# Performance work log

Measured on AMD Instinct MI355X. Metric: run time of the kernel, lower is better.

## Reference

```python
import jax, jax.numpy as jnp
import numpy as np

BN_EPS = 1e-5


def setup_inputs() -> dict:
    key = jax.random.key(0)
    ks = jax.random.split(key, 10)
    B, C, N = 16, 512, 4096
    Cr = C // 4
    s = 0.05
    return {
        "x": jax.random.normal(ks[0], (B, C, N), dtype=jnp.float32),
        # channel attention MLP (1x1 convs on pooled vector)
        "w1": jax.random.normal(ks[1], (Cr, C), dtype=jnp.float32) * s,
        "b1": jnp.zeros((Cr,), jnp.float32),
        "w2": jax.random.normal(ks[2], (C, Cr), dtype=jnp.float32) * s,
        "b2": jnp.zeros((C,), jnp.float32),
        # spatial attention branch
        "w3": jax.random.normal(ks[3], (Cr, C), dtype=jnp.float32) * s,
        "b3": jnp.zeros((Cr,), jnp.float32),
        "bn_gamma": jnp.ones((Cr,), jnp.float32),
        "bn_beta": jnp.zeros((Cr,), jnp.float32),
        "bn_mean": jnp.zeros((Cr,), jnp.float32),
        "bn_var": jnp.ones((Cr,), jnp.float32),
        "w4": jax.random.normal(ks[4], (1, Cr), dtype=jnp.float32) * s,
        "b4": jnp.zeros((1,), jnp.float32),
    }


def reference(x, w1, b1, w2, b2, w3, b3, bn_gamma, bn_beta, bn_mean, bn_var, w4, b4):
    # x: [B, C, N]; inference semantics (Dropout = identity, BN uses running stats)
    # ---- channel attention ----
    pooled = jnp.mean(x, axis=-1)                        # [B, C] (AdaptiveAvgPool1d(1))
    h = jax.nn.relu(pooled @ w1.T + b1)                  # [B, C/4]
    ca = jax.nn.sigmoid(h @ w2.T + b2)[:, :, None]       # [B, C, 1]
    x_ca = x * ca                                        # [B, C, N]
    # ---- spatial attention ----
    h2 = jnp.einsum('oc,bcn->bon', w3, x_ca) + b3[:, None]    # [B, C/4, N]
    inv = bn_gamma / jnp.sqrt(bn_var + BN_EPS)                 # [C/4]
    h2 = h2 * inv[:, None] + (bn_beta - bn_mean * inv)[:, None]
    h2 = jax.nn.relu(h2)
    sa = jax.nn.sigmoid(jnp.einsum('oc,bcn->bon', w4, h2) + b4[:, None])  # [B, 1, N]
    return x + x_ca * sa
```

## Files before the change

### kernel.cpp

```cpp
#include <hip/hip_runtime.h>
#include <math.h>

constexpr int B  = 16;
constexpr int C  = 512;
constexpr int N  = 4096;
constexpr int CR = 128;
constexpr int NT = 128;
constexpr int KC = 64;

typedef __attribute__((ext_vector_type(8))) short bf16x8;
typedef __attribute__((ext_vector_type(4))) float f32x4;

__device__ __forceinline__ float sigmoidf_(float v) {
    return 1.0f / (1.0f + __expf(-v));
}
__device__ __forceinline__ unsigned f2bf(float f) {
    unsigned u = __float_as_uint(f);
    u += 0x7fffu + ((u >> 16) & 1u);
    return u >> 16;
}

#define LGKM_BARRIER() do {                                   \
    asm volatile("s_waitcnt lgkmcnt(0)" ::: "memory");        \
    __builtin_amdgcn_s_barrier();                             \
    asm volatile("" ::: "memory");                            \
} while (0)

__global__ __launch_bounds__(256) void k_pre(
    const float* __restrict__ x, float* __restrict__ pooled,
    const float* __restrict__ w3, const float* __restrict__ b3,
    const float* __restrict__ gamma, const float* __restrict__ beta,
    const float* __restrict__ mean, const float* __restrict__ var,
    unsigned short* __restrict__ w3f, float* __restrict__ bias2)
{
    if (blockIdx.x < 2048) {
        int w    = threadIdx.x >> 6;
        int lane = threadIdx.x & 63;
        int row  = blockIdx.x * 4 + w;
        const float4* xr = (const float4*)(x + (size_t)row * N);
        float s = 0.f;
        #pragma unroll
        for (int i = 0; i < 16; ++i) {
            float4 v = xr[i * 64 + lane];
            s += v.x + v.y + v.z + v.w;
        }
        #pragma unroll
        for (int off = 32; off; off >>= 1) s += __shfl_xor(s, off, 64);
        if (lane == 0) pooled[row] = s * (1.0f / N);
    } else {
        int idx  = (blockIdx.x - 2048) * 256 + threadIdx.x;
        int g    = idx >> 6;
        int lane = idx & 63;
        int ck   = g >> 4;
        int kk   = (g >> 3) & 1;
        int ob   = g & 7;
        int o    = ob * 16 + (lane & 15);
        int c    = ck * 64 + kk * 32 + (lane >> 4) * 8;
        float inv = gamma[o] * rsqrtf(var[o] + 1e-5f);
        float4 a  = *(const float4*)(w3 + o * C + c);
        float4 bq = *(const float4*)(w3 + o * C + c + 4);
        unsigned r0 = f2bf(a.x * inv)  | (f2bf(a.y * inv) << 16);
        unsigned r1 = f2bf(a.z * inv)  | (f2bf(a.w * inv) << 16);
        unsigned r2 = f2bf(bq.x * inv) | (f2bf(bq.y * inv) << 16);
        unsigned r3 = f2bf(bq.z * inv) | (f2bf(bq.w * inv) << 16);
        *(uint4*)((char*)w3f + (size_t)idx * 16) = make_uint4(r0, r1, r2, r3);
        if (idx < CR) {
            float iv = gamma[idx] * rsqrtf(var[idx] + 1e-5f);
            bias2[idx] = b3[idx] * iv + beta[idx] - mean[idx] * iv;
        }
    }
}

__global__ __launch_bounds__(128) void k_ca(
    const float* __restrict__ pooled,
    const float* __restrict__ w1, const float* __restrict__ b1,
    const float* __restrict__ w2, const float* __restrict__ b2,
    float* __restrict__ ca)
{
    __shared__ float ps[C];
    __shared__ float hs[CR];
    int b = blockIdx.x, t = threadIdx.x;
    #pragma unroll
    for (int i = 0; i < 4; ++i) ps[t + i * 128] = pooled[b * C + t + i * 128];
    __syncthreads();

    float acc = b1[t];
    const float4* wr = (const float4*)(w1 + t * C);
    const float4* pr = (const float4*)ps;
    #pragma unroll 4
    for (int i = 0; i < C / 4; ++i) {
        float4 wv = wr[i], pv = pr[i];
        acc += wv.x * pv.x + wv.y * pv.y + wv.z * pv.z + wv.w * pv.w;
    }
    hs[t] = fmaxf(acc, 0.f);
    __syncthreads();

    #pragma unroll
    for (int k = 0; k < 4; ++k) {
        int c2 = t + k * 128;
        float a = b2[c2];
        const float4* w2r = (const float4*)(w2 + c2 * CR);
        const float4* hr  = (const float4*)hs;
        #pragma unroll 4
        for (int i = 0; i < CR / 4; ++i) {
            float4 wv = w2r[i], hv = hr[i];
            a += wv.x * hv.x + wv.y * hv.y + wv.z * hv.z + wv.w * hv.w;
        }
        ca[b * C + c2] = sigmoidf_(a);
    }
}

__global__ __launch_bounds__(512, 2) void k_main(
    const float* __restrict__ x, const float* __restrict__ ca,
    const unsigned short* __restrict__ w3f, const float* __restrict__ bias2,
    const float* __restrict__ w4, const float* __restrict__ b4,
    float* __restrict__ out)
{
    __shared__ __align__(16) short lds_x[2][NT * KC];
    __shared__ float ca_s[C];
    __shared__ __align__(16) float sa_s[NT];
    __shared__ float red[4][NT];
    __shared__ float bias2_s[CR];
    __shared__ float w4_s[CR];

    const int t    = threadIdx.x;
    const int lane = t & 63;
    const int w    = t >> 6;
    const int b    = blockIdx.y;
    const int n0   = blockIdx.x * NT;
    const int wo   = (w & 3) * 32;
    const int wn   = (w >> 2) * 64;
    const int ob0  = (w & 3) * 2;

    const size_t xbase = (size_t)b * C * N + n0;
    const int ng = t & 63;
    const int cg = t >> 6;

    float2 xva[8], xvb[8];

#define LOADX(dst, CK) do { const int c0_ = (CK) * KC;                         \
    _Pragma("unroll") for (int ci = 0; ci < 8; ++ci)                           \
        dst[ci] = *(const float2*)(x + xbase + (size_t)(c0_ + cg * 8 + ci) * N + 2 * ng); \
} while (0)

#define CONVERT_WRITE(src, CK, BUF) do { const int c0_ = (CK) * KC;            \
    unsigned q0[4], q1[4];                                                     \
    _Pragma("unroll") for (int h = 0; h < 4; ++h) {                            \
        float s0 = ca_s[c0_ + cg * 8 + 2 * h];                                 \
        float s1 = ca_s[c0_ + cg * 8 + 2 * h + 1];                             \
        q0[h] = f2bf(src[2 * h].x * s0) | (f2bf(src[2 * h + 1].x * s1) << 16); \
        q1[h] = f2bf(src[2 * h].y * s0) | (f2bf(src[2 * h + 1].y * s1) << 16); \
    }                                                                          \
    int nl0 = 2 * ng, nl1 = 2 * ng + 1;                                        \
    int a0 = (nl0 * 128 + cg * 16) ^ ((nl0 & 7) << 4);                         \
    int a1 = (nl1 * 128 + cg * 16) ^ ((nl1 & 7) << 4);                         \
    *(uint4*)((char*)lds_x[BUF] + a0) = make_uint4(q0[0], q0[1], q0[2], q0[3]);\
    *(uint4*)((char*)lds_x[BUF] + a1) = make_uint4(q1[0], q1[1], q1[2], q1[3]);\
} while (0)

    LOADX(xva, 0);
    LOADX(xvb, 1);

    ca_s[t] = ca[b * C + t];
    if (t < CR) { bias2_s[t] = bias2[t]; w4_s[t] = w4[t]; }
    LGKM_BARRIER();

    CONVERT_WRITE(xva, 0, 0);

    f32x4 acc[2][4];
    #pragma unroll
    for (int i = 0; i < 2; ++i)
        #pragma unroll
        for (int j = 0; j < 4; ++j) acc[i][j] = (f32x4)0.f;

    const char* wf = (const char*)w3f;

    #pragma unroll
    for (int ck = 0; ck < 8; ++ck) {
        if (ck < 6) { if (ck & 1) LOADX(xvb, ck + 2); else LOADX(xva, ck + 2); }

        LGKM_BARRIER();

        #pragma unroll
        for (int kk = 0; kk < 2; ++kk) {
            bf16x8 af[2];
            #pragma unroll
            for (int i = 0; i < 2; ++i) {
                int g = ck * 16 + kk * 8 + ob0 + i;
                af[i] = *(const bf16x8*)(wf + (size_t)(g * 64 + lane) * 16);
            }
            bf16x8 bfr[4];
            #pragma unroll
            for (int j = 0; j < 4; ++j) {
                int br = wn + j * 16 + (lane & 15);
                int bb = (br * 128 + kk * 64 + (lane >> 4) * 16) ^ ((br & 7) << 4);
                bfr[j] = *(const bf16x8*)((const char*)lds_x[ck & 1] + bb);
            }
            #pragma unroll
            for (int i = 0; i < 2; ++i)
                #pragma unroll
                for (int j = 0; j < 4; ++j)
                    acc[i][j] = __builtin_amdgcn_mfma_f32_16x16x32_bf16(af[i], bfr[j], acc[i][j], 0, 0, 0);
        }
        if (ck < 7) { if (ck & 1) CONVERT_WRITE(xva, ck + 1, 0); else CONVERT_WRITE(xvb, ck + 1, 1); }
    }

    #pragma unroll
    for (int j = 0; j < 4; ++j) {
        float p = 0.f;
        #pragma unroll
        for (int i = 0; i < 2; ++i) {
            #pragma unroll
            for (int r = 0; r < 4; ++r) {
                int o = wo + i * 16 + ((lane >> 4) << 2) + r;
                p = fmaf(w4_s[o], fmaxf(acc[i][j][r] + bias2_s[o], 0.f), p);
            }
        }
        p += __shfl_xor(p, 16, 64);
        p += __shfl_xor(p, 32, 64);
        if (lane < 16) red[w & 3][wn + j * 16 + lane] = p;
    }
    __syncthreads();
    if (t < NT) sa_s[t] = sigmoidf_(red[0][t] + red[1][t] + red[2][t] + red[3][t] + b4[0]);
    __syncthreads();

    #pragma unroll 4
    for (int it = 0; it < 32; ++it) {
        int f4 = it * 512 + t;
        int c  = f4 >> 5;
        int n4 = f4 & 31;
        size_t off = xbase + (size_t)c * N + n4 * 4;
        float4 v = *(const float4*)(x + off);
        float cav = ca_s[c];
        float4 sv = *(const float4*)&sa_s[n4 * 4];
        float4 o4;
        o4.x = v.x * fmaf(cav, sv.x, 1.0f);
        o4.y = v.y * fmaf(cav, sv.y, 1.0f);
        o4.z = v.z * fmaf(cav, sv.z, 1.0f);
        o4.w = v.w * fmaf(cav, sv.w, 1.0f);
        *(float4*)(out + off) = o4;
    }
#undef LOADX
#undef CONVERT_WRITE
}

extern "C" void kernel_launch(void* const* d_in, const int* in_sizes, int n_in,
                              void* d_out, int out_size, void* d_ws, size_t ws_size,
                              hipStream_t stream)
{
    const float* x   = (const float*)d_in[0];
    const float* w1  = (const float*)d_in[1];
    const float* b1  = (const float*)d_in[2];
    const float* w2  = (const float*)d_in[3];
    const float* b2  = (const float*)d_in[4];
    const float* w3  = (const float*)d_in[5];
    const float* b3  = (const float*)d_in[6];
    const float* g   = (const float*)d_in[7];
    const float* be  = (const float*)d_in[8];
    const float* mn  = (const float*)d_in[9];
    const float* vr  = (const float*)d_in[10];
    const float* w4  = (const float*)d_in[11];
    const float* b4  = (const float*)d_in[12];
    float* out = (float*)d_out;

    float* ws     = (float*)d_ws;
    float* pooled = ws;
    float* ca     = ws + 8192;
    float* bias2  = ws + 16384;
    unsigned short* w3f = (unsigned short*)(ws + 16640);

    k_pre<<<2048 + 32, 256, 0, stream>>>(x, pooled, w3, b3, g, be, mn, vr, w3f, bias2);
    k_ca<<<B, 128, 0, stream>>>(pooled, w1, b1, w2, b2, ca);
    dim3 g3(N / NT, B);
    k_main<<<g3, 512, 0, stream>>>(x, ca, w3f, bias2, w4, b4, out);
}
```

Baseline: 121.2 us.

## Fold channel attention into per-batch W3 and split output pass into separate kernel

The channel-attention scale is folded into a per-batch bf16 copy of the BN-scaled W3 inside k_ca, so the GEMM kernel converts raw x to bf16 without multiplying by ca. The final elementwise output pass moves out of the GEMM kernel into a separate streaming kernel that reads a stored sa vector. This removes per-element ca multiplies and LDS lookups from the GEMM inner loop and frees the GEMM kernel from the output tail. In exchange it adds a kernel launch, a 2 MB per-batch weight buffer, and an extra sa round trip through global memory. The bf16 rounding order also changes slightly.

```diff
diff --git a/kernel.cpp b/kernel.cpp
--- a/kernel.cpp
+++ b/kernel.cpp
@@ -71,33 +71,37 @@
     }
 }
 
-__global__ __launch_bounds__(128) void k_ca(
+__global__ __launch_bounds__(256) void k_ca(
     const float* __restrict__ pooled,
     const float* __restrict__ w1, const float* __restrict__ b1,
     const float* __restrict__ w2, const float* __restrict__ b2,
-    float* __restrict__ ca)
+    const unsigned short* __restrict__ w3f,
+    float* __restrict__ ca, unsigned short* __restrict__ w3b)
 {
     __shared__ float ps[C];
     __shared__ float hs[CR];
+    __shared__ float ca_s[C];
     int b = blockIdx.x, t = threadIdx.x;
+    ps[t] = pooled[b * C + t];
+    ps[t + 256] = pooled[b * C + t + 256];
+    __syncthreads();
+
+    if (t < CR) {
+        float acc = b1[t];
+        const float4* wr = (const float4*)(w1 + t * C);
+        const float4* pr = (const float4*)ps;
+        #pragma unroll 4
+        for (int i = 0; i < C / 4; ++i) {
+            float4 wv = wr[i], pv = pr[i];
+            acc += wv.x * pv.x + wv.y * pv.y + wv.z * pv.z + wv.w * pv.w;
+        }
+        hs[t] = fmaxf(acc, 0.f);
+    }
+    __syncthreads();
+
     #pragma unroll
-    for (int i = 0; i < 4; ++i) ps[t + i * 128] = pooled[b * C + t + i * 128];
-    __syncthreads();
-
-    float acc = b1[t];
-    const float4* wr = (const float4*)(w1 + t * C);
-    const float4* pr = (const float4*)ps;
-    #pragma unroll 4
-    for (int i = 0; i < C / 4; ++i) {
-        float4 wv = wr[i], pv = pr[i];
-        acc += wv.x * pv.x + wv.y * pv.y + wv.z * pv.z + wv.w * pv.w;
-    }
-    hs[t] = fmaxf(acc, 0.f);
-    __syncthreads();
-
-    #pragma unroll
-    for (int k = 0; k < 4; ++k) {
-        int c2 = t + k * 128;
+    for (int k = 0; k < 2; ++k) {
+        int c2 = t + k * 256;
         float a = b2[c2];
         const float4* w2r = (const float4*)(w2 + c2 * CR);
         const float4* hr  = (const float4*)hs;
@@ -106,19 +110,49 @@
             float4 wv = w2r[i], hv = hr[i];
             a += wv.x * hv.x + wv.y * hv.y + wv.z * hv.z + wv.w * hv.w;
         }
-        ca[b * C + c2] = sigmoidf_(a);
-    }
-}
-
-__global__ __launch_bounds__(512, 2) void k_main(
-    const float* __restrict__ x, const float* __restrict__ ca,
-    const unsigned short* __restrict__ w3f, const float* __restrict__ bias2,
-    const float* __restrict__ w4, const float* __restrict__ b4,
-    float* __restrict__ out)
+        float cav = sigmoidf_(a);
+        ca_s[c2] = cav;
+        ca[b * C + c2] = cav;
+    }
+    __syncthreads();
+
+    #pragma unroll 4
+    for (int j = 0; j < 32; ++j) {
+        int i    = j * 256 + t;
+        int g    = i >> 6;
+        int lane = i & 63;
+        int ck   = g >> 4;
+        int kk   = (g >> 3) & 1;
+        int c0   = ck * 64 + kk * 32 + ((lane >> 4) << 3);
+        uint4 wv = *(const uint4*)((const char*)w3f + (size_t)i * 16);
+        const float* cb = &ca_s[c0];
+        uint4 ov;
+        {
+            float lo = __uint_as_float(wv.x << 16), hi = __uint_as_float(wv.x & 0xffff0000u);
+            ov.x = f2bf(lo * cb[0]) | (f2bf(hi * cb[1]) << 16);
+        }
+        {
+            float lo = __uint_as_float(wv.y << 16), hi = __uint_as_float(wv.y & 0xffff0000u);
+            ov.y = f2bf(lo * cb[2]) | (f2bf(hi * cb[3]) << 16);
+        }
+        {
+            float lo = __uint_as_float(wv.z << 16), hi = __uint_as_float(wv.z & 0xffff0000u);
+            ov.z = f2bf(lo * cb[4]) | (f2bf(hi * cb[5]) << 16);
+        }
+        {
+            float lo = __uint_as_float(wv.w << 16), hi = __uint_as_float(wv.w & 0xffff0000u);
+            ov.w = f2bf(lo * cb[6]) | (f2bf(hi * cb[7]) << 16);
+        }
+        *(uint4*)((char*)w3b + ((size_t)b * 8192 + i) * 16) = ov;
+    }
+}
+
+__global__ __launch_bounds__(512, 2) void k_gemm(
+    const float* __restrict__ x, const unsigned short* __restrict__ w3b,
+    const float* __restrict__ bias2, const float* __restrict__ w4,
+    const float* __restrict__ b4, float* __restrict__ sa)
 {
     __shared__ __align__(16) short lds_x[2][NT * KC];
-    __shared__ float ca_s[C];
-    __shared__ __align__(16) float sa_s[NT];
     __shared__ float red[4][NT];
     __shared__ float bias2_s[CR];
     __shared__ float w4_s[CR];
@@ -136,6 +170,8 @@
     const int ng = t & 63;
     const int cg = t >> 6;
 
+    if (t < CR) { bias2_s[t] = bias2[t]; w4_s[t] = w4[t]; }
+
     float2 xva[8], xvb[8];
 
 #define LOADX(dst, CK) do { const int c0_ = (CK) * KC;                         \
@@ -143,13 +179,11 @@
         dst[ci] = *(const float2*)(x + xbase + (size_t)(c0_ + cg * 8 + ci) * N + 2 * ng); \
 } while (0)
 
-#define CONVERT_WRITE(src, CK, BUF) do { const int c0_ = (CK) * KC;            \
+#define CONVERT_WRITE(src, BUF) do {                                           \
     unsigned q0[4], q1[4];                                                     \
     _Pragma("unroll") for (int h = 0; h < 4; ++h) {                            \
-        float s0 = ca_s[c0_ + cg * 8 + 2 * h];                                 \
-        float s1 = ca_s[c0_ + cg * 8 + 2 * h + 1];                             \
-        q0[h] = f2bf(src[2 * h].x * s0) | (f2bf(src[2 * h + 1].x * s1) << 16); \
-        q1[h] = f2bf(src[2 * h].y * s0) | (f2bf(src[2 * h + 1].y * s1) << 16); \
+        q0[h] = f2bf(src[2 * h].x) | (f2bf(src[2 * h + 1].x) << 16);           \
+        q1[h] = f2bf(src[2 * h].y) | (f2bf(src[2 * h + 1].y) << 16);           \
     }                                                                          \
     int nl0 = 2 * ng, nl1 = 2 * ng + 1;                                        \
     int a0 = (nl0 * 128 + cg * 16) ^ ((nl0 & 7) << 4);                         \
@@ -160,12 +194,7 @@
 
     LOADX(xva, 0);
     LOADX(xvb, 1);
-
-    ca_s[t] = ca[b * C + t];
-    if (t < CR) { bias2_s[t] = bias2[t]; w4_s[t] = w4[t]; }
-    LGKM_BARRIER();
-
-    CONVERT_WRITE(xva, 0, 0);
+    CONVERT_WRITE(xva, 0);
 
     f32x4 acc[2][4];
     #pragma unroll
@@ -173,7 +202,7 @@
         #pragma unroll
         for (int j = 0; j < 4; ++j) acc[i][j] = (f32x4)0.f;
 
-    const char* wf = (const char*)w3f;
+    const char* wb = (const char*)w3b + (size_t)b * 131072;
 
     #pragma unroll
     for (int ck = 0; ck < 8; ++ck) {
@@ -187,7 +216,7 @@
             #pragma unroll
             for (int i = 0; i < 2; ++i) {
                 int g = ck * 16 + kk * 8 + ob0 + i;
-                af[i] = *(const bf16x8*)(wf + (size_t)(g * 64 + lane) * 16);
+                af[i] = *(const bf16x8*)(wb + (size_t)(g * 64 + lane) * 16);
             }
             bf16x8 bfr[4];
             #pragma unroll
@@ -202,7 +231,7 @@
                 for (int j = 0; j < 4; ++j)
                     acc[i][j] = __builtin_amdgcn_mfma_f32_16x16x32_bf16(af[i], bfr[j], acc[i][j], 0, 0, 0);
         }
-        if (ck < 7) { if (ck & 1) CONVERT_WRITE(xva, ck + 1, 0); else CONVERT_WRITE(xvb, ck + 1, 1); }
+        if (ck < 7) { if (ck & 1) CONVERT_WRITE(xva, 0); else CONVERT_WRITE(xvb, 1); }
     }
 
     #pragma unroll
@@ -221,27 +250,36 @@
         if (lane < 16) red[w & 3][wn + j * 16 + lane] = p;
     }
     __syncthreads();
-    if (t < NT) sa_s[t] = sigmoidf_(red[0][t] + red[1][t] + red[2][t] + red[3][t] + b4[0]);
-    __syncthreads();
-
-    #pragma unroll 4
-    for (int it = 0; it < 32; ++it) {
-        int f4 = it * 512 + t;
-        int c  = f4 >> 5;
-        int n4 = f4 & 31;
-        size_t off = xbase + (size_t)c * N + n4 * 4;
-        float4 v = *(const float4*)(x + off);
-        float cav = ca_s[c];
-        float4 sv = *(const float4*)&sa_s[n4 * 4];
-        float4 o4;
-        o4.x = v.x * fmaf(cav, sv.x, 1.0f);
-        o4.y = v.y * fmaf(cav, sv.y, 1.0f);
-        o4.z = v.z * fmaf(cav, sv.z, 1.0f);
-        o4.w = v.w * fmaf(cav, sv.w, 1.0f);
-        *(float4*)(out + off) = o4;
-    }
+    if (t < NT)
+        sa[b * N + n0 + t] = sigmoidf_(red[0][t] + red[1][t] + red[2][t] + red[3][t] + b4[0]);
 #undef LOADX
 #undef CONVERT_WRITE
+}
+
+__global__ __launch_bounds__(256) void k_out(
+    const float* __restrict__ x, const float* __restrict__ ca,
+    const float* __restrict__ sa, float* __restrict__ out)
+{
+    const float4* x4  = (const float4*)x;
+    const float4* sa4 = (const float4*)sa;
+    float4* o4        = (float4*)out;
+    int base = blockIdx.x * 256 + threadIdx.x;
+    #pragma unroll 4
+    for (int it = 0; it < 16; ++it) {
+        int i4 = base + it * 524288;
+        float4 v  = x4[i4];
+        int b  = i4 >> 19;
+        int c  = (i4 >> 10) & 511;
+        int n4 = i4 & 1023;
+        float cav = ca[b * 512 + c];
+        float4 sv = sa4[b * 1024 + n4];
+        float4 r;
+        r.x = v.x * fmaf(cav, sv.x, 1.0f);
+        r.y = v.y * fmaf(cav, sv.y, 1.0f);
+        r.z = v.z * fmaf(cav, sv.z, 1.0f);
+        r.w = v.w * fmaf(cav, sv.w, 1.0f);
+        o4[i4] = r;
+    }
 }
 
 extern "C" void kernel_launch(void* const* d_in, const int* in_sizes, int n_in,
@@ -268,9 +306,12 @@
     float* ca     = ws + 8192;
     float* bias2  = ws + 16384;
     unsigned short* w3f = (unsigned short*)(ws + 16640);
+    unsigned short* w3b = (unsigned short*)(ws + 49408);
+    float* sa     = ws + 573696;
 
     k_pre<<<2048 + 32, 256, 0, stream>>>(x, pooled, w3, b3, g, be, mn, vr, w3f, bias2);
-    k_ca<<<B, 128, 0, stream>>>(pooled, w1, b1, w2, b2, ca);
+    k_ca<<<B, 256, 0, stream>>>(pooled, w1, b1, w2, b2, w3f, ca, w3b);
     dim3 g3(N / NT, B);
-    k_main<<<g3, 512, 0, stream>>>(x, ca, w3f, bias2, w4, b4, out);
-}
+    k_gemm<<<g3, 512, 0, stream>>>(x, w3b, bias2, w4, b4, sa);
+    k_out<<<2048, 256, 0, stream>>>(x, ca, sa, out);
+}
```

New measurement: 124.9 us, median of 2. 3.0% more time.

## Fold channel attention into per-batch weights and pre-transpose x to bf16

Applied to the files above, without the earlier changes.

The pooling pass now also writes a transposed bf16 copy of x laid out in MFMA fragment order. The channel-attention kernel folds the ca scale into a per-batch copy of the bf16 w3 weights. The main GEMM then streams both operands straight from global memory, with no LDS staging or per-tile conversion, and targets higher occupancy. This trades an extra 64 MB write plus a re-read of that buffer for removing the in-loop x conversion and barriers. A fallback path is kept for when the workspace is too small.

```diff
diff --git a/kernel.cpp b/kernel.cpp
--- a/kernel.cpp
+++ b/kernel.cpp
@@ -31,24 +31,51 @@
     const float* __restrict__ w3, const float* __restrict__ b3,
     const float* __restrict__ gamma, const float* __restrict__ beta,
     const float* __restrict__ mean, const float* __restrict__ var,
-    unsigned short* __restrict__ w3f, float* __restrict__ bias2)
+    unsigned short* __restrict__ w3f, float* __restrict__ bias2,
+    unsigned short* __restrict__ xbT, int do_xbt)
 {
-    if (blockIdx.x < 2048) {
-        int w    = threadIdx.x >> 6;
-        int lane = threadIdx.x & 63;
-        int row  = blockIdx.x * 4 + w;
-        const float4* xr = (const float4*)(x + (size_t)row * N);
-        float s = 0.f;
-        #pragma unroll
-        for (int i = 0; i < 16; ++i) {
-            float4 v = xr[i * 64 + lane];
-            s += v.x + v.y + v.z + v.w;
-        }
-        #pragma unroll
-        for (int off = 32; off; off >>= 1) s += __shfl_xor(s, off, 64);
-        if (lane == 0) pooled[row] = s * (1.0f / N);
+    if (blockIdx.x < 512) {
+        __shared__ float tr[16][256];
+        const int g = blockIdx.x, b = g >> 5, c16 = g & 31;
+        const int t = threadIdx.x, lane = t & 63, w = t >> 6;
+        const float4* xr = (const float4*)(x + ((size_t)b * C + c16 * 16) * N);
+        float ps[4] = {0.f, 0.f, 0.f, 0.f};
+        for (int ch = 0; ch < 16; ++ch) {
+            float4 v[4];
+            #pragma unroll
+            for (int i = 0; i < 4; ++i) {
+                int r = i * 4 + w;
+                v[i] = xr[(size_t)r * 1024 + ch * 64 + lane];
+                ps[i] += v[i].x + v[i].y + v[i].z + v[i].w;
+            }
+            if (do_xbt) {
+                #pragma unroll
+                for (int i = 0; i < 4; ++i)
+                    *(float4*)&tr[i * 4 + w][lane * 4] = v[i];
+                __syncthreads();
+                int n = ch * 256 + t;
+                unsigned q[8];
+                #pragma unroll
+                for (int h = 0; h < 8; ++h)
+                    q[h] = f2bf(tr[2 * h][t]) | (f2bf(tr[2 * h + 1][t]) << 16);
+                size_t off = (((size_t)b * 32 + c16) * 4096 + n) * 16;
+                *(uint4*)(xbT + off)     = make_uint4(q[0], q[1], q[2], q[3]);
+                *(uint4*)(xbT + off + 8) = make_uint4(q[4], q[5], q[6], q[7]);
+                __syncthreads();
+            }
+        }
+        #pragma unroll
+        for (int i = 0; i < 4; ++i) {
+            #pragma unroll
+            for (int o = 32; o; o >>= 1) ps[i] += __shfl_xor(ps[i], o, 64);
+        }
+        if (lane == 0) {
+            #pragma unroll
+            for (int i = 0; i < 4; ++i)
+                pooled[b * C + c16 * 16 + i * 4 + w] = ps[i] * (1.0f / N);
+        }
     } else {
-        int idx  = (blockIdx.x - 2048) * 256 + threadIdx.x;
+        int idx  = (blockIdx.x - 512) * 256 + threadIdx.x;
         int g    = idx >> 6;
         int lane = idx & 63;
         int ck   = g >> 4;
@@ -71,33 +98,37 @@
     }
 }
 
-__global__ __launch_bounds__(128) void k_ca(
+__global__ __launch_bounds__(256) void k_ca(
     const float* __restrict__ pooled,
     const float* __restrict__ w1, const float* __restrict__ b1,
     const float* __restrict__ w2, const float* __restrict__ b2,
-    float* __restrict__ ca)
+    const unsigned short* __restrict__ w3f,
+    float* __restrict__ ca, unsigned short* __restrict__ w3b)
 {
     __shared__ float ps[C];
     __shared__ float hs[CR];
+    __shared__ float ca_s[C];
     int b = blockIdx.x, t = threadIdx.x;
-    #pragma unroll
-    for (int i = 0; i < 4; ++i) ps[t + i * 128] = pooled[b * C + t + i * 128];
-    __syncthreads();
-
-    float acc = b1[t];
-    const float4* wr = (const float4*)(w1 + t * C);
-    const float4* pr = (const float4*)ps;
-    #pragma unroll 4
-    for (int i = 0; i < C / 4; ++i) {
-        float4 wv = wr[i], pv = pr[i];
-        acc += wv.x * pv.x + wv.y * pv.y + wv.z * pv.z + wv.w * pv.w;
-    }
-    hs[t] = fmaxf(acc, 0.f);
-    __syncthreads();
-
-    #pragma unroll
-    for (int k = 0; k < 4; ++k) {
-        int c2 = t + k * 128;
+    ps[t] = pooled[b * C + t];
+    ps[t + 256] = pooled[b * C + t + 256];
+    __syncthreads();
+
+    if (t < CR) {
+        float acc = b1[t];
+        const float4* wr = (const float4*)(w1 + t * C);
+        const float4* pr = (const float4*)ps;
+        #pragma unroll 4
+        for (int i = 0; i < C / 4; ++i) {
+            float4 wv = wr[i], pv = pr[i];
+            acc += wv.x * pv.x + wv.y * pv.y + wv.z * pv.z + wv.w * pv.w;
+        }
+        hs[t] = fmaxf(acc, 0.f);
+    }
+    __syncthreads();
+
+    #pragma unroll
+    for (int k = 0; k < 2; ++k) {
+        int c2 = t + k * 256;
         float a = b2[c2];
         const float4* w2r = (const float4*)(w2 + c2 * CR);
         const float4* hr  = (const float4*)hs;
@@ -106,20 +137,52 @@
             float4 wv = w2r[i], hv = hr[i];
             a += wv.x * hv.x + wv.y * hv.y + wv.z * hv.z + wv.w * hv.w;
         }
-        ca[b * C + c2] = sigmoidf_(a);
-    }
-}
-
-__global__ __launch_bounds__(512, 2) void k_main(
-    const float* __restrict__ x, const float* __restrict__ ca,
-    const unsigned short* __restrict__ w3f, const float* __restrict__ bias2,
-    const float* __restrict__ w4, const float* __restrict__ b4,
-    float* __restrict__ out)
+        float cav = sigmoidf_(a);
+        ca_s[c2] = cav;
+        ca[b * C + c2] = cav;
+    }
+    __syncthreads();
+
+    #pragma unroll 4
+    for (int j = 0; j < 32; ++j) {
+        int i    = j * 256 + t;
+        int g    = i >> 6;
+        int lane = i & 63;
+        int ck   = g >> 4;
+        int kk   = (g >> 3) & 1;
+        int c0   = ck * 64 + kk * 32 + ((lane >> 4) << 3);
+        uint4 wv = *(const uint4*)((const char*)w3f + (size_t)i * 16);
+        const float* cb = &ca_s[c0];
+        uint4 ov;
+        {
+            float lo = __uint_as_float(wv.x << 16), hi = __uint_as_float(wv.x & 0xffff0000u);
+            ov.x = f2bf(lo * cb[0]) | (f2bf(hi * cb[1]) << 16);
+        }
+        {
+            float lo = __uint_as_float(wv.y << 16), hi = __uint_as_float(wv.y & 0xffff0000u);
+            ov.y = f2bf(lo * cb[2]) | (f2bf(hi * cb[3]) << 16);
+        }
+        {
+            float lo = __uint_as_float(wv.z << 16), hi = __uint_as_float(wv.z & 0xffff0000u);
+            ov.z = f2bf(lo * cb[4]) | (f2bf(hi * cb[5]) << 16);
+        }
+        {
+            float lo = __uint_as_float(wv.w << 16), hi = __uint_as_float(wv.w & 0xffff0000u);
+            ov.w = f2bf(lo * cb[6]) | (f2bf(hi * cb[7]) << 16);
+        }
+        *(uint4*)((char*)w3b + ((size_t)b * 8192 + i) * 16) = ov;
+    }
+}
+
+__global__ __launch_bounds__(512, 4) void k_gemm_out(
+    const float* __restrict__ x, const unsigned short* __restrict__ xbT,
+    const unsigned short* __restrict__ w3b, const float* __restrict__ ca,
+    const float* __restrict__ bias2, const float* __restrict__ w4,
+    const float* __restrict__ b4, float* __restrict__ out)
 {
-    __shared__ __align__(16) short lds_x[2][NT * KC];
+    __shared__ float red[4][NT];
+    __shared__ __align__(16) float sa_s[NT];
     __shared__ float ca_s[C];
-    __shared__ __align__(16) float sa_s[NT];
-    __shared__ float red[4][NT];
     __shared__ float bias2_s[CR];
     __shared__ float w4_s[CR];
 
@@ -132,40 +195,15 @@
     const int wn   = (w >> 2) * 64;
     const int ob0  = (w & 3) * 2;
 
-    const size_t xbase = (size_t)b * C * N + n0;
-    const int ng = t & 63;
-    const int cg = t >> 6;
-
-    float2 xva[8], xvb[8];
-
-#define LOADX(dst, CK) do { const int c0_ = (CK) * KC;                         \
-    _Pragma("unroll") for (int ci = 0; ci < 8; ++ci)                           \
-        dst[ci] = *(const float2*)(x + xbase + (size_t)(c0_ + cg * 8 + ci) * N + 2 * ng); \
-} while (0)
-
-#define CONVERT_WRITE(src, CK, BUF) do { const int c0_ = (CK) * KC;            \
-    unsigned q0[4], q1[4];                                                     \
-    _Pragma("unroll") for (int h = 0; h < 4; ++h) {                            \
-        float s0 = ca_s[c0_ + cg * 8 + 2 * h];                                 \
-        float s1 = ca_s[c0_ + cg * 8 + 2 * h + 1];                             \
-        q0[h] = f2bf(src[2 * h].x * s0) | (f2bf(src[2 * h + 1].x * s1) << 16); \
-        q1[h] = f2bf(src[2 * h].y * s0) | (f2bf(src[2 * h + 1].y * s1) << 16); \
-    }                                                                          \
-    int nl0 = 2 * ng, nl1 = 2 * ng + 1;                                        \
-    int a0 = (nl0 * 128 + cg * 16) ^ ((nl0 & 7) << 4);                         \
-    int a1 = (nl1 * 128 + cg * 16) ^ ((nl1 & 7) << 4);                         \
-    *(uint4*)((char*)lds_x[BUF] + a0) = make_uint4(q0[0], q0[1], q0[2], q0[3]);\
-    *(uint4*)((char*)lds_x[BUF] + a1) = make_uint4(q1[0], q1[1], q1[2], q1[3]);\
-} while (0)
-
-    LOADX(xva, 0);
-    LOADX(xvb, 1);
-
-    ca_s[t] = ca[b * C + t];
-    if (t < CR) { bias2_s[t] = bias2[t]; w4_s[t] = w4[t]; }
-    LGKM_BARRIER();
-
-    CONVERT_WRITE(xva, 0, 0);
+    if (t < 256) { ca_s[t] = ca[b * C + t]; ca_s[t + 256] = ca[b * C + t + 256]; }
+    if (t < CR)  { bias2_s[t] = bias2[t]; w4_s[t] = w4[t]; }
+
+    const int csel = lane >> 4;
+    const unsigned short* bbase = xbT
+        + ((size_t)b * 32 + (csel >> 1)) * 65536
+        + (size_t)(n0 + wn + (lane & 15)) * 16
+        + (csel & 1) * 8;
+    const char* wb = (const char*)w3b + (size_t)b * 131072 + (size_t)lane * 16;
 
     f32x4 acc[2][4];
     #pragma unroll
@@ -173,36 +211,27 @@
         #pragma unroll
         for (int j = 0; j < 4; ++j) acc[i][j] = (f32x4)0.f;
 
-    const char* wf = (const char*)w3f;
-
     #pragma unroll
     for (int ck = 0; ck < 8; ++ck) {
-        if (ck < 6) { if (ck & 1) LOADX(xvb, ck + 2); else LOADX(xva, ck + 2); }
-
-        LGKM_BARRIER();
-
-        #pragma unroll
-        for (int kk = 0; kk < 2; ++kk) {
-            bf16x8 af[2];
-            #pragma unroll
-            for (int i = 0; i < 2; ++i) {
-                int g = ck * 16 + kk * 8 + ob0 + i;
-                af[i] = *(const bf16x8*)(wf + (size_t)(g * 64 + lane) * 16);
-            }
-            bf16x8 bfr[4];
-            #pragma unroll
-            for (int j = 0; j < 4; ++j) {
-                int br = wn + j * 16 + (lane & 15);
-                int bb = (br * 128 + kk * 64 + (lane >> 4) * 16) ^ ((br & 7) << 4);
-                bfr[j] = *(const bf16x8*)((const char*)lds_x[ck & 1] + bb);
-            }
+        bf16x8 af[2][2];
+        #pragma unroll
+        for (int kk = 0; kk < 2; ++kk)
+            #pragma unroll
+            for (int i = 0; i < 2; ++i)
+                af[kk][i] = *(const bf16x8*)(wb + (size_t)(ck * 16 + kk * 8 + ob0 + i) * 1024);
+        bf16x8 bfv[2][4];
+        #pragma unroll
+        for (int kk = 0; kk < 2; ++kk)
+            #pragma unroll
+            for (int j = 0; j < 4; ++j)
+                bfv[kk][j] = *(const bf16x8*)(bbase + (size_t)(ck * 4 + kk * 2) * 65536 + j * 256);
+        #pragma unroll
+        for (int kk = 0; kk < 2; ++kk)
             #pragma unroll
             for (int i = 0; i < 2; ++i)
                 #pragma unroll
                 for (int j = 0; j < 4; ++j)
-                    acc[i][j] = __builtin_amdgcn_mfma_f32_16x16x32_bf16(af[i], bfr[j], acc[i][j], 0, 0, 0);
-        }
-        if (ck < 7) { if (ck & 1) CONVERT_WRITE(xva, ck + 1, 0); else CONVERT_WRITE(xvb, ck + 1, 1); }
+                    acc[i][j] = __builtin_amdgcn_mfma_f32_16x16x32_bf16(af[kk][i], bfv[kk][j], acc[i][j], 0, 0, 0);
     }
 
     #pragma unroll
@@ -221,9 +250,11 @@
         if (lane < 16) red[w & 3][wn + j * 16 + lane] = p;
     }
     __syncthreads();
-    if (t < NT) sa_s[t] = sigmoidf_(red[0][t] + red[1][t] + red[2][t] + red[3][t] + b4[0]);
-    __syncthreads();
-
+    if (t < NT)
+        sa_s[t] = sigmoidf_(red[0][t] + red[1][t] + red[2][t] + red[3][t] + b4[0]);
+    __syncthreads();
+
+    const size_t xbase = (size_t)b * C * N + n0;
     #pragma unroll 4
     for (int it = 0; it < 32; ++it) {
         int f4 = it * 512 + t;
@@ -240,8 +271,136 @@
         o4.w = v.w * fmaf(cav, sv.w, 1.0f);
         *(float4*)(out + off) = o4;
     }
+}
+
+__global__ __launch_bounds__(512, 2) void k_main_fb(
+    const float* __restrict__ x, const float* __restrict__ ca,
+    const unsigned short* __restrict__ w3f, const float* __restrict__ bias2,
+    const float* __restrict__ w4, const float* __restrict__ b4,
+    float* __restrict__ out)
+{
+    __shared__ __align__(16) short lds_x[2][NT * KC];
+    __shared__ float ca_s[C];
+    __shared__ __align__(16) float sa_s[NT];
+    __shared__ float red[4][NT];
+    __shared__ float bias2_s[CR];
+    __shared__ float w4_s[CR];
+
+    const int t    = threadIdx.x;
+    const int lane = t & 63;
+    const int w    = t >> 6;
+    const int b    = blockIdx.y;
+    const int n0   = blockIdx.x * NT;
+    const int wo   = (w & 3) * 32;
+    const int wn   = (w >> 2) * 64;
+    const int ob0  = (w & 3) * 2;
+
+    const size_t xbase = (size_t)b * C * N + n0;
+    const int ng = t & 63;
+    const int cg = t >> 6;
+
+    ca_s[t] = ca[b * C + t];
+    if (t < CR) { bias2_s[t] = bias2[t]; w4_s[t] = w4[t]; }
+
+    float2 xva[8], xvb[8];
+
+#define LOADX(dst, CK) do { const int c0_ = (CK) * KC;                         \
+    _Pragma("unroll") for (int ci = 0; ci < 8; ++ci)                           \
+        dst[ci] = *(const float2*)(x + xbase + (size_t)(c0_ + cg * 8 + ci) * N + 2 * ng); \
+} while (0)
+#define CONVERT_WRITE(src, CK, BUF) do { const int c0_ = (CK) * KC;            \
+    unsigned q0[4], q1[4];                                                     \
+    _Pragma("unroll") for (int h = 0; h < 4; ++h) {                            \
+        float s0 = ca_s[c0_ + cg * 8 + 2 * h];                                 \
+        float s1 = ca_s[c0_ + cg * 8 + 2 * h + 1];                             \
+        q0[h] = f2bf(src[2 * h].x * s0) | (f2bf(src[2 * h + 1].x * s1) << 16); \
+        q1[h] = f2bf(src[2 * h].y * s0) | (f2bf(src[2 * h + 1].y * s1) << 16); \
+    }                                                                          \
+    int nl0 = 2 * ng, nl1 = 2 * ng + 1;                                        \
+    int a0 = (nl0 * 128 + cg * 16) ^ ((nl0 & 7) << 4);                         \
+    int a1 = (nl1 * 128 + cg * 16) ^ ((nl1 & 7) << 4);                         \
+    *(uint4*)((char*)lds_x[BUF] + a0) = make_uint4(q0[0], q0[1], q0[2], q0[3]);\
+    *(uint4*)((char*)lds_x[BUF] + a1) = make_uint4(q1[0], q1[1], q1[2], q1[3]);\
+} while (0)
+
+    LOADX(xva, 0);
+    LOADX(xvb, 1);
+    LGKM_BARRIER();
+    CONVERT_WRITE(xva, 0, 0);
+
+    f32x4 acc[2][4];
+    #pragma unroll
+    for (int i = 0; i < 2; ++i)
+        #pragma unroll
+        for (int j = 0; j < 4; ++j) acc[i][j] = (f32x4)0.f;
+
+    const char* wf = (const char*)w3f;
+
+    #pragma unroll
+    for (int ck = 0; ck < 8; ++ck) {
+        if (ck < 6) { if (ck & 1) LOADX(xvb, ck + 2); else LOADX(xva, ck + 2); }
+        LGKM_BARRIER();
+        #pragma unroll
+        for (int kk = 0; kk < 2; ++kk) {
+            bf16x8 af[2];
+            #pragma unroll
+            for (int i = 0; i < 2; ++i) {
+                int g = ck * 16 + kk * 8 + ob0 + i;
+                af[i] = *(const bf16x8*)(wf + (size_t)(g * 64 + lane) * 16);
+            }
+            bf16x8 bfr[4];
+            #pragma unroll
+            for (int j = 0; j < 4; ++j) {
+                int br = wn + j * 16 + (lane & 15);
+                int bb = (br * 128 + kk * 64 + (lane >> 4) * 16) ^ ((br & 7) << 4);
+                bfr[j] = *(const bf16x8*)((const char*)lds_x[ck & 1] + bb);
+            }
+            #pragma unroll
+            for (int i = 0; i < 2; ++i)
+                #pragma unroll
+                for (int j = 0; j < 4; ++j)
+                    acc[i][j] = __builtin_amdgcn_mfma_f32_16x16x32_bf16(af[i], bfr[j], acc[i][j], 0, 0, 0);
+        }
+        if (ck < 7) { if (ck & 1) CONVERT_WRITE(xva, ck + 1, 0); else CONVERT_WRITE(xvb, ck + 1, 1); }
+    }
 #undef LOADX
 #undef CONVERT_WRITE
+
+    #pragma unroll
+    for (int j = 0; j < 4; ++j) {
+        float p = 0.f;
+        #pragma unroll
+        for (int i = 0; i < 2; ++i) {
+            #pragma unroll
+            for (int r = 0; r < 4; ++r) {
+                int o = wo + i * 16 + ((lane >> 4) << 2) + r;
+                p = fmaf(w4_s[o], fmaxf(acc[i][j][r] + bias2_s[o], 0.f), p);
+            }
+        }
+        p += __shfl_xor(p, 16, 64);
+        p += __shfl_xor(p, 32, 64);
+        if (lane < 16) red[w & 3][wn + j * 16 + lane] = p;
+    }
+    __syncthreads();
+    if (t < NT) sa_s[t] = sigmoidf_(red[0][t] + red[1][t] + red[2][t] + red[3][t] + b4[0]);
+    __syncthreads();
+
+    #pragma unroll 4
+    for (int it = 0; it < 32; ++it) {
+        int f4 = it * 512 + t;
+        int c  = f4 >> 5;
+        int n4 = f4 & 31;
+        size_t off = xbase + (size_t)c * N + n4 * 4;
+        float4 v = *(const float4*)(x + off);
+        float cav = ca_s[c];
+        float4 sv = *(const float4*)&sa_s[n4 * 4];
+        float4 o4;
+        o4.x = v.x * fmaf(cav, sv.x, 1.0f);
+        o4.y = v.y * fmaf(cav, sv.y, 1.0f);
+        o4.z = v.z * fmaf(cav, sv.z, 1.0f);
+        o4.w = v.w * fmaf(cav, sv.w, 1.0f);
+        *(float4*)(out + off) = o4;
+    }
 }
 
 extern "C" void kernel_launch(void* const* d_in, const int* in_sizes, int n_in,
@@ -268,9 +427,18 @@
     float* ca     = ws + 8192;
     float* bias2  = ws + 16384;
     unsigned short* w3f = (unsigned short*)(ws + 16640);
-
-    k_pre<<<2048 + 32, 256, 0, stream>>>(x, pooled, w3, b3, g, be, mn, vr, w3f, bias2);
-    k_ca<<<B, 128, 0, stream>>>(pooled, w1, b1, w2, b2, ca);
+    unsigned short* w3b = (unsigned short*)(ws + 49408);
+    unsigned short* xbT = (unsigned short*)(ws + 573696);
+
+    const size_t need = (size_t)573696 * 4 + (size_t)B * C * N * 2;
+    const int use_xbt = (ws_size >= need) ? 1 : 0;
+
+    k_pre<<<512 + 32, 256, 0, stream>>>(x, pooled, w3, b3, g, be, mn, vr,
+                                        w3f, bias2, xbT, use_xbt);
+    k_ca<<<B, 256, 0, stream>>>(pooled, w1, b1, w2, b2, w3f, ca, w3b);
     dim3 g3(N / NT, B);
-    k_main<<<g3, 512, 0, stream>>>(x, ca, w3f, bias2, w4, b4, out);
-}
+    if (use_xbt)
+        k_gemm_out<<<g3, 512, 0, stream>>>(x, xbT, w3b, ca, bias2, w4, b4, out);
+    else
+        k_main_fb<<<g3, 512, 0, stream>>>(x, ca, w3f, bias2, w4, b4, out);
+}
```

Result: slower. 157.6 us (+30.0%).
